# Kernel optimization log

Measured on AMD Instinct MI355X. Metric: run time of the kernel, lower is better.

Reference implementation:

```python
import jax, jax.numpy as jnp
import numpy as np

K = 20          # neighbors
M = 8           # weight-bank size per layer
EPS = 1e-5      # BatchNorm eps


def _bn(x, axes):
    # training-mode BatchNorm at init (gamma=1, beta=0), biased variance like torch
    mu = x.mean(axes, keepdims=True)
    var = x.var(axes, keepdims=True)
    return (x - mu) * jax.lax.rsqrt(var + EPS)


def _gather(feat, idx):
    # feat [B,N,C], idx [B,N,K] -> neighbor features [B,N,K,C]
    return jax.vmap(lambda f, i: f[i])(feat, idx)


def _knn_idx(x):
    # x [B,C,N]; pairwise_distance = -||xi||^2 + 2 xi.xj - ||xj||^2 (neg sq dist)
    sq = jnp.sum(x * x, axis=1)                      # [B,N]
    inner = jnp.einsum('bcn,bcm->bnm', x, x)          # [B,N,N]
    pd = 2.0 * inner - sq[:, :, None] - sq[:, None, :]
    return jax.lax.top_k(pd, K)[1]                    # [B,N,K]


def _scorenet(xyz, w1, w2, b):
    # xyz [B,N,K,6]; 1x1 Conv2d == channel-last matmul; BN2d over (B,N,K)
    h = jax.nn.relu(_bn(xyz @ w1, (0, 1, 2)))         # [B,N,K,16]
    s = h @ w2 + b                                    # [B,N,K,M]
    return jax.nn.softmax(s, axis=-1) + 0.5           # softmax over m, bias=0.5


def _paconv(feat, idx, ker, score):
    # feat [B,N,C]; ker [2C, M*O]; score [B,N,K,M]
    # torch: point = concat(x,x) @ ker -> [B,N,M,O]; center = x @ ker[:C]
    # assemble_dgcnn (assign_score_withk, aggregate='sum'):
    #   out[b,n,o] = sum_{k,m} score[b,n,k,m] * (point[b, idx[b,n,k], m, o] - center[b, n, m, o])
    C = feat.shape[-1]
    k3 = ker.reshape(2 * C, M, -1)
    Wa, Wb = k3[:C], k3[C:]                           # point uses Wa+Wb (x repeated); center uses Wa
    nf = _gather(feat, idx)                           # [B,N,K,C]
    T = jnp.einsum('bnkm,bnkc->bnmc', score, nf)      # score-weighted neighbor feats
    out = jnp.einsum('bnmc,cmo->bno', T, Wa + Wb)
    out = out - jnp.einsum('bnm,bnc,cmo->bno', score.sum(2), feat, Wa)
    return jax.nn.relu(_bn(out, (0, 1)))              # BN1d over (B,N), channel-last


def setup_inputs() -> dict:
    key = jax.random.key(0)
    ks = jax.random.split(key, 18)
    B, N = 32, 1024
    dims = [(3, 64), (64, 64), (64, 128), (128, 256)]
    d = {"x": jax.random.normal(ks[0], (B, 3, N), dtype=jnp.float32)}
    for i, (ci, co) in enumerate(dims):
        scale = (2.0 / (2 * ci)) ** 0.5  # kaiming_normal over fan_in=2*ci
        d[f"mat{i+1}"] = jax.random.normal(ks[1 + i], (2 * ci, M * co), dtype=jnp.float32) * scale
        d[f"sn{i+1}_w1"] = jax.random.normal(ks[5 + i], (6, 16), dtype=jnp.float32) * 0.4
        d[f"sn{i+1}_w2"] = jax.random.normal(ks[9 + i], (16, M), dtype=jnp.float32) * 0.25
        d[f"sn{i+1}_b"] = jnp.zeros((M,), dtype=jnp.float32)
    d["conv5_w"] = jax.random.normal(ks[13], (512, 1024), dtype=jnp.float32) * 0.04
    d["lin1_w"] = jax.random.normal(ks[14], (2048, 512), dtype=jnp.float32) * 0.02
    d["lin2_w"] = jax.random.normal(ks[15], (512, 256), dtype=jnp.float32) * 0.04
    d["lin3_w"] = jax.random.normal(ks[16], (256, 40), dtype=jnp.float32) * 0.06
    d["lin3_b"] = jnp.zeros((40,), dtype=jnp.float32)
    return d


def reference(x, mat1, mat2, mat3, mat4,
              sn1_w1, sn1_w2, sn1_b, sn2_w1, sn2_w2, sn2_b,
              sn3_w1, sn3_w2, sn3_b, sn4_w1, sn4_w2, sn4_b,
              conv5_w, lin1_w, lin2_w, lin3_w, lin3_b):
    idx = _knn_idx(x)                                  # [B,N,K]
    xT = jnp.swapaxes(x, 1, 2)                         # [B,N,3]
    nx = _gather(xT, idx)                              # [B,N,K,3]
    xyz = jnp.concatenate([nx - xT[:, :, None, :], nx], axis=-1)  # [B,N,K,6]

    p1 = _paconv(xT, idx, mat1, _scorenet(xyz, sn1_w1, sn1_w2, sn1_b))  # [B,N,64]
    p2 = _paconv(p1, idx, mat2, _scorenet(xyz, sn2_w1, sn2_w2, sn2_b))  # [B,N,64]
    p3 = _paconv(p2, idx, mat3, _scorenet(xyz, sn3_w1, sn3_w2, sn3_b))  # [B,N,128]
    p4 = _paconv(p3, idx, mat4, _scorenet(xyz, sn4_w1, sn4_w2, sn4_b))  # [B,N,256]

    p = jnp.concatenate([p1, p2, p3, p4], axis=-1)     # [B,N,512]
    p = jax.nn.relu(_bn(p @ conv5_w, (0, 1)))          # [B,N,1024]
    g = jnp.concatenate([p.max(axis=1), p.mean(axis=1)], axis=-1)  # [B,2048]
    h = jax.nn.relu(_bn(g @ lin1_w, (0,)))             # [B,512] (dropout = identity)
    h = jax.nn.relu(_bn(h @ lin2_w, (0,)))             # [B,256]
    return h @ lin3_w + lin3_b                         # [B,40]
```

## Files before the change

### kernel.cpp

```cpp
#include <hip/hip_runtime.h>
#include <cstdint>
#include <cstddef>

static constexpr int Bc  = 32;
static constexpr int Nc  = 1024;
static constexpr int Kc  = 20;
static constexpr int Mc  = 8;
static constexpr int BNc = Bc * Nc;
static constexpr int BNKc = BNc * Kc;

typedef __attribute__((ext_vector_type(4))) float f32x4;
typedef _Float16 f16x8 __attribute__((ext_vector_type(8)));

__device__ inline short f2h(float v) { _Float16 h = (_Float16)v; return __builtin_bit_cast(short, h); }
__device__ inline float h2f(short s) { return (float)__builtin_bit_cast(_Float16, s); }

__global__ void zero_kernel(float* p, int n) {
  int gid = blockIdx.x * blockDim.x + threadIdx.x;
  if (gid < n) p[gid] = 0.f;
}

__global__ __launch_bounds__(256) void knn_kernel(const float* __restrict__ x,
                                                  int* __restrict__ idxout) {
  int wv = threadIdx.x >> 6;
  int bn = blockIdx.x * 4 + wv;
  int b = bn >> 10, n = bn & (Nc - 1);
  int lane = threadIdx.x & 63;
  const float* xb = x + (size_t)b * 3 * Nc;
  float cx = xb[n], cy = xb[Nc + n], cz = xb[2 * Nc + n];
  float sqc = cx * cx + cy * cy + cz * cz;
  float d[16];
#pragma unroll
  for (int j = 0; j < 16; j++) {
    int m2 = j * 64 + lane;
    float xm = xb[m2], ym = xb[Nc + m2], zm = xb[2 * Nc + m2];
    d[j] = 2.f * (cx * xm + cy * ym + cz * zm) - sqc - (xm * xm + ym * ym + zm * zm);
  }
  int* out = idxout + (size_t)bn * Kc;
  for (int kk = 0; kk < Kc; kk++) {
    float bd = d[0]; int bj = 0;
#pragma unroll
    for (int j = 1; j < 16; j++)
      if (d[j] > bd) { bd = d[j]; bj = j; }
    int bm = bj * 64 + lane;
#pragma unroll
    for (int off = 32; off; off >>= 1) {
      float od = __shfl_down(bd, off);
      int   om = __shfl_down(bm, off);
      if (od > bd || (od == bd && om < bm)) { bd = od; bm = om; }
    }
    bm = __shfl(bm, 0);
    if (lane == 0) out[kk] = bm;
    int bmj = bm >> 6;
    bool mine = (bm & 63) == lane;
#pragma unroll
    for (int j = 0; j < 16; j++)
      if (mine && j == bmj) d[j] = -3e38f;
  }
}

__global__ __launch_bounds__(256) void xt_kernel(const float* __restrict__ x,
                                                 float* __restrict__ xT) {
  int gid = blockIdx.x * blockDim.x + threadIdx.x;
  int c = gid % 3;
  int bn = gid / 3;
  int b = bn >> 10, n = bn & (Nc - 1);
  xT[gid] = x[((size_t)b * 3 + c) * Nc + n];
}

__device__ inline void xyz_at(const float* __restrict__ xT, const int* __restrict__ idx,
                              int e, float v[6]) {
  int bn = e / Kc;
  int b = bn >> 10;
  int nb = idx[e];
  const float* pc = xT + (size_t)bn * 3;
  const float* pn = xT + ((size_t)(b << 10) + nb) * 3;
#pragma unroll
  for (int c = 0; c < 3; c++) { float nv = pn[c]; v[c] = nv - pc[c]; v[3 + c] = nv; }
}

__global__ __launch_bounds__(256) void xyz_stats_kernel(const float* __restrict__ xT,
                                                        const int* __restrict__ idx,
                                                        float* __restrict__ accum) {
  __shared__ float sPart[4 * 42];
  int tid = threadIdx.x;
  int gid = blockIdx.x * 256 + tid;
  float a[42];
#pragma unroll
  for (int t = 0; t < 42; t++) a[t] = 0.f;
  for (int i = 0; i < 8; i++) {
    float v[6];
    xyz_at(xT, idx, gid + i * 81920, v);
#pragma unroll
    for (int c = 0; c < 6; c++) a[c] += v[c];
    int t = 6;
#pragma unroll
    for (int c = 0; c < 6; c++)
#pragma unroll
      for (int d = 0; d < 6; d++) a[t++] += v[c] * v[d];
  }
  int lane = tid & 63, wid = tid >> 6;
#pragma unroll
  for (int t = 0; t < 42; t++) {
    float v = a[t];
#pragma unroll
    for (int off = 32; off; off >>= 1) v += __shfl_down(v, off);
    if (lane == 0) sPart[wid * 42 + t] = v;
  }
  __syncthreads();
  if (tid < 42) {
    float s = sPart[tid] + sPart[42 + tid] + sPart[84 + tid] + sPart[126 + tid];
    atomicAdd(&accum[tid], s);
  }
}

__global__ void snstats_kernel(const float* __restrict__ accum,
                               const float* __restrict__ w1a, const float* __restrict__ w1b,
                               const float* __restrict__ w1c, const float* __restrict__ w1d,
                               float* __restrict__ snstats) {
  int t = threadIdx.x;
  int l = t >> 4, j = t & 15;
  const float* w1 = (l == 0) ? w1a : (l == 1) ? w1b : (l == 2) ? w1c : w1d;
  const float invc = 1.f / (float)BNKc;
  float wj[6];
  float mu = 0.f;
#pragma unroll
  for (int c = 0; c < 6; c++) { wj[c] = w1[c * 16 + j]; mu += accum[c] * invc * wj[c]; }
  float e2 = 0.f;
#pragma unroll
  for (int c = 0; c < 6; c++)
#pragma unroll
    for (int d = 0; d < 6; d++) e2 += wj[c] * wj[d] * (accum[6 + c * 6 + d] * invc);
  float var = e2 - mu * mu;
  snstats[t * 2] = mu;
  snstats[t * 2 + 1] = rsqrtf(var + 1e-5f);
}

__global__ __launch_bounds__(256) void score4_kernel(
    const float* __restrict__ xT, const int* __restrict__ idx,
    const float* __restrict__ w1a, const float* __restrict__ w2a, const float* __restrict__ b1,
    const float* __restrict__ w1b, const float* __restrict__ w2b, const float* __restrict__ b2,
    const float* __restrict__ w1c, const float* __restrict__ w2c, const float* __restrict__ b3,
    const float* __restrict__ w1d, const float* __restrict__ w2d, const float* __restrict__ b4,
    const float* __restrict__ snst, short* __restrict__ score4) {
  __shared__ float sW1[4][96], sW2[4][128], sB[4][8], sMu[4][16], sRs[4][16];
  int tid = threadIdx.x;
  if (tid < 96) { sW1[0][tid] = w1a[tid]; sW1[1][tid] = w1b[tid]; sW1[2][tid] = w1c[tid]; sW1[3][tid] = w1d[tid]; }
  else if (tid < 224) { int t = tid - 96; sW2[0][t] = w2a[t]; sW2[1][t] = w2b[t]; sW2[2][t] = w2c[t]; sW2[3][t] = w2d[t]; }
  else if (tid < 232) { int t = tid - 224; sB[0][t] = b1[t]; sB[1][t] = b2[t]; sB[2][t] = b3[t]; sB[3][t] = b4[t]; }
  else if (tid < 248) {
    int t = tid - 232;
#pragma unroll
    for (int l = 0; l < 4; l++) { sMu[l][t] = snst[(l * 16 + t) * 2]; sRs[l][t] = snst[(l * 16 + t) * 2 + 1]; }
  }
  __syncthreads();
  int e = blockIdx.x * 256 + tid;
  float v[6];
  xyz_at(xT, idx, e, v);
#pragma unroll
  for (int l = 0; l < 4; l++) {
    float h[16];
#pragma unroll
    for (int j = 0; j < 16; j++) {
      float a = 0.f;
#pragma unroll
      for (int c = 0; c < 6; c++) a += v[c] * sW1[l][c * 16 + j];
      a = (a - sMu[l][j]) * sRs[l][j];
      h[j] = a > 0.f ? a : 0.f;
    }
    float s[8];
    float mx = -3e38f;
#pragma unroll
    for (int m = 0; m < 8; m++) {
      float a = sB[l][m];
#pragma unroll
      for (int j = 0; j < 16; j++) a += h[j] * sW2[l][j * 8 + m];
      s[m] = a;
      mx = fmaxf(mx, a);
    }
    float sum = 0.f;
#pragma unroll
    for (int m = 0; m < 8; m++) { s[m] = expf(s[m] - mx); sum += s[m]; }
    float inv = 1.f / sum;
    short* op = score4 + (size_t)l * BNKc * 8 + (size_t)e * 8;
#pragma unroll
    for (int m = 0; m < 8; m++) op[m] = f2h(s[m] * inv + 0.5f);
  }
}

template <int C, int Co, int MH>
__global__ __launch_bounds__(256) void paconv_kernel(
    const float* __restrict__ feat, int fstride,
    const float* __restrict__ ker,
    const short* __restrict__ score,
    const int* __restrict__ idx,
    float* __restrict__ outp, int ostride) {
  constexpr int PT = 8;
  constexpr int MS = Mc / MH;
  __shared__ float sX[PT][2 * MH * C];
  __shared__ float sSc[PT * Kc * Mc];
  __shared__ int sIdx[PT * Kc];
  __shared__ float sFc[PT][C];
  __shared__ float sSum[PT][Mc];

  int tid = threadIdx.x;
  int pbase = blockIdx.x * PT;
  int bN = pbase & ~(Nc - 1);

  for (int e = tid; e < PT * Kc; e += 256) sIdx[e] = idx[(size_t)pbase * Kc + e];
  for (int e = tid; e < PT * Kc * Mc; e += 256) sSc[e] = h2f(score[(size_t)pbase * Kc * Mc + e]);
  for (int e = tid; e < PT * C; e += 256) {
    int p = e / C, c = e - p * C;
    sFc[p][c] = feat[(size_t)(pbase + p) * fstride + c];
  }
  __syncthreads();
  for (int e = tid; e < PT * Mc; e += 256) {
    int p = e >> 3, m = e & 7;
    float s = 0.f;
#pragma unroll
    for (int k = 0; k < Kc; k++) s += sSc[p * Kc * Mc + k * Mc + m];
    sSum[p][m] = s;
  }
  __syncthreads();

  constexpr int OG = Co;
  constexpr int PG = 256 / OG;
  constexpr int PPT = PT / PG;
  int o = tid % OG;
  int pg = tid / OG;
  float acc[PPT];
#pragma unroll
  for (int i = 0; i < PPT; i++) acc[i] = 0.f;

  for (int ms = 0; ms < MS; ms++) {
    int mb = ms * MH;
    for (int e = tid; e < PT * C; e += 256) {
      int p = e / C, c = e - p * C;
      float t[MH];
#pragma unroll
      for (int mm = 0; mm < MH; mm++) t[mm] = 0.f;
      const float* sc = &sSc[p * Kc * Mc + mb];
      for (int k = 0; k < Kc; k++) {
        float v = feat[(size_t)(bN + sIdx[p * Kc + k]) * fstride + c];
#pragma unroll
        for (int mm = 0; mm < MH; mm++) t[mm] += sc[k * Mc + mm] * v;
      }
      float fc = sFc[p][c];
#pragma unroll
      for (int mm = 0; mm < MH; mm++) {
        sX[p][mm * C + c] = t[mm] - sSum[p][mb + mm] * fc;
        sX[p][MH * C + mm * C + c] = t[mm];
      }
    }
    __syncthreads();
#pragma unroll
    for (int mm = 0; mm < MH; mm++) {
      int m = mb + mm;
      const float* kerm = ker + (size_t)m * Co + o;
      for (int c = 0; c < C; c++) {
        float wA = kerm[(size_t)c * (Mc * Co)];
        float wB = kerm[(size_t)(C + c) * (Mc * Co)];
        int r = mm * C + c;
#pragma unroll
        for (int i = 0; i < PPT; i++) {
          int p = pg * PPT + i;
          acc[i] += sX[p][r] * wA;
          acc[i] += sX[p][MH * C + r] * wB;
        }
      }
    }
    __syncthreads();
  }

#pragma unroll
  for (int i = 0; i < PPT; i++) {
    int p = pg * PPT + i;
    outp[(size_t)(pbase + p) * ostride + o] = acc[i];
  }
}

template <int C>
__global__ __launch_bounds__(256) void gather_kernel(
    const short* __restrict__ pb, int coff,
    const short* __restrict__ score,
    const int* __restrict__ idx,
    short* __restrict__ T, short* __restrict__ sumb) {
  constexpr int PT = 256 / C;
  constexpr int KH = Mc * C;
  __shared__ float sSc[PT][Kc][Mc];
  __shared__ int   sIdx[PT][Kc];
  int tid = threadIdx.x;
  int pbase = blockIdx.x * PT;
  int bbase = pbase & ~(Nc - 1);
  for (int e = tid; e < PT * Kc * Mc; e += 256) (&sSc[0][0][0])[e] = h2f(score[(size_t)pbase * Kc * Mc + e]);
  for (int e = tid; e < PT * Kc; e += 256) (&sIdx[0][0])[e] = idx[(size_t)pbase * Kc + e];
  __syncthreads();
  if (tid < PT * Mc) {
    int p = tid >> 3, m = tid & 7;
    float s = 0.f;
#pragma unroll
    for (int k = 0; k < Kc; k++) s += sSc[p][k][m];
    sumb[(size_t)(pbase + p) * 8 + m] = f2h(s);
  }
  int p = tid / C, c = tid - p * C;
  float t[Mc];
#pragma unroll
  for (int m = 0; m < Mc; m++) t[m] = 0.f;
  for (int k = 0; k < Kc; k++) {
    float v = h2f(pb[(size_t)(bbase + sIdx[p][k]) * 512 + coff + c]);
#pragma unroll
    for (int m = 0; m < Mc; m++) t[m] += sSc[p][k][m] * v;
  }
  short* rowp = T + (size_t)(pbase + p) * KH;
#pragma unroll
  for (int m = 0; m < Mc; m++) rowp[m * C + c] = f2h(t[m]);
}

__global__ __launch_bounds__(256) void kerconv_all_kernel(
    const float* __restrict__ m2, const float* __restrict__ m3,
    const float* __restrict__ m4, const float* __restrict__ w5,
    short* __restrict__ kb) {
  int gid = blockIdx.x * 256 + threadIdx.x;
  const float* ker; short* dst; int C, Co, g;
  if (gid < 65536)       { ker = m2; dst = kb;          C = 64;  Co = 64;  g = gid; }
  else if (gid < 196608) { ker = m3; dst = kb + 65536;  C = 64;  Co = 128; g = gid - 65536; }
  else if (gid < 720896) { ker = m4; dst = kb + 196608; C = 128; Co = 256; g = gid - 196608; }
  else {
    int g5 = gid - 720896;
    int o = g5 >> 9, k = g5 & 511;
    kb[720896 + g5] = f2h(w5[(size_t)k * 1024 + o]);
    return;
  }
  int KH = Mc * C, K2 = 2 * KH;
  int o = g / K2, r = g - o * K2;
  float v;
  if (r < KH) {
    int m = r / C, c = r - m * C;
    v = ker[(size_t)c * (Mc * Co) + m * Co + o] + ker[(size_t)(C + c) * (Mc * Co) + m * Co + o];
  } else {
    int r2 = r - KH;
    int m = r2 / C, c = r2 - m * C;
    v = -ker[(size_t)c * (Mc * Co) + m * Co + o];
  }
  dst[g] = f2h(v);
}

template <int BM, int BN, bool OUT_HALF>
__global__ __launch_bounds__(256) void gemm_kernel(
    const short* __restrict__ A,
    const short* __restrict__ Bt,
    int K,
    void* __restrict__ Cout, int ldc) {
  constexpr int BK = 64;
  constexpr int FN = BN / 32;
  constexpr int FMW = BM / 32;
  __shared__ short sA[BM * BK];
  __shared__ short sB[BN * BK];
  int tid = threadIdx.x;
  int lane = tid & 63, wv = tid >> 6;
  int wrow = (wv & 1) * (BM / 2);
  int wcol = (wv >> 1) * (BN / 2);
  int bm0 = blockIdx.x * BM;
  int bn0 = blockIdx.y * BN;
  int r15 = lane & 15, quad = lane >> 4;
  int swz = r15 & 7;

  f32x4 acc[FMW][FN];
#pragma unroll
  for (int fm = 0; fm < FMW; fm++)
#pragma unroll
    for (int fn = 0; fn < FN; fn++) acc[fm][fn] = (f32x4){0.f, 0.f, 0.f, 0.f};

  for (int k0 = 0; k0 < K; k0 += BK) {
#pragma unroll
    for (int i = 0; i < (BM * BK / 8) / 256; i++) {
      int cb = i * 256 + wv * 64;
      int chunk = cb + lane;
      int row = chunk >> 3, kc = (chunk & 7) ^ (row & 7);
      const short* g = A + (size_t)(bm0 + row) * K + k0 + kc * 8;
      __builtin_amdgcn_global_load_lds((const __attribute__((address_space(1))) void*)g,
                                       (__attribute__((address_space(3))) void*)&sA[cb * 8],
                                       16, 0, 0);
    }
#pragma unroll
    for (int i = 0; i < (BN * BK / 8) / 256; i++) {
      int cb = i * 256 + wv * 64;
      int chunk = cb + lane;
      int row = chunk >> 3, kc = (chunk & 7) ^ (row & 7);
      const short* g = Bt + (size_t)(bn0 + row) * K + k0 + kc * 8;
      __builtin_amdgcn_global_load_lds((const __attribute__((address_space(1))) void*)g,
                                       (__attribute__((address_space(3))) void*)&sB[cb * 8],
                                       16, 0, 0);
    }
    __syncthreads();
#pragma unroll
    for (int kk = 0; kk < BK; kk += 32) {
      f16x8 af[FMW], bf[FN];
      int ccol = (kk >> 3) + quad;
#pragma unroll
      for (int fm = 0; fm < FMW; fm++)
        af[fm] = *(const f16x8*)&sA[(wrow + fm * 16 + r15) * BK + ((ccol ^ swz) * 8)];
#pragma unroll
      for (int fn = 0; fn < FN; fn++)
        bf[fn] = *(const f16x8*)&sB[(wcol + fn * 16 + r15) * BK + ((ccol ^ swz) * 8)];
#pragma unroll
      for (int fm = 0; fm < FMW; fm++)
#pragma unroll
        for (int fn = 0; fn < FN; fn++)
          acc[fm][fn] = __builtin_amdgcn_mfma_f32_16x16x32_f16(af[fm], bf[fn], acc[fm][fn], 0, 0, 0);
    }
    __syncthreads();
  }

#pragma unroll
  for (int fn = 0; fn < FN; fn++) {
    int col = bn0 + wcol + fn * 16 + r15;
#pragma unroll
    for (int fm = 0; fm < FMW; fm++) {
      int rowb = bm0 + wrow + fm * 16 + quad * 4;
#pragma unroll
      for (int r = 0; r < 4; r++) {
        float v = acc[fm][fn][r];
        if constexpr (OUT_HALF) ((short*)Cout)[(size_t)(rowb + r) * ldc + col] = f2h(v);
        else                    ((float*)Cout)[(size_t)(rowb + r) * ldc + col] = v;
      }
    }
  }
}

template <int BM, int BN, int C>
__global__ __launch_bounds__(256) void gemm_r1_kernel(
    const short* __restrict__ T,
    const short* __restrict__ Bt,
    const short* __restrict__ pb, int coff,
    const short* __restrict__ sumb,
    short* __restrict__ Cout, int ldc) {
  constexpr int BK = 64;
  constexpr int KH = Mc * C;
  constexpr int K2 = 2 * KH;
  constexpr int FN = BN / 32;
  constexpr int FMW = BM / 32;
  __shared__ short sA[BM * BK];
  __shared__ short sB[BN * BK];
  __shared__ short sFc[BM * C];
  __shared__ short sSm[BM * 8];
  int tid = threadIdx.x;
  int lane = tid & 63, wv = tid >> 6;
  int wrow = (wv & 1) * (BM / 2);
  int wcol = (wv >> 1) * (BN / 2);
  int bm0 = blockIdx.x * BM;
  int bn0 = blockIdx.y * BN;
  int r15 = lane & 15, quad = lane >> 4;
  int swz = r15 & 7;

  for (int e = tid; e < BM * C; e += 256) {
    int p = e / C, c = e - p * C;
    sFc[e] = pb[(size_t)(bm0 + p) * 512 + coff + c];
  }
  for (int e = tid; e < BM * 8; e += 256) sSm[e] = sumb[(size_t)bm0 * 8 + e];

  f32x4 acc[FMW][FN];
#pragma unroll
  for (int fm = 0; fm < FMW; fm++)
#pragma unroll
    for (int fn = 0; fn < FN; fn++) acc[fm][fn] = (f32x4){0.f, 0.f, 0.f, 0.f};
  __syncthreads();

  for (int k0 = 0; k0 < K2; k0 += BK) {
    if (k0 < KH) {
#pragma unroll
      for (int i = 0; i < (BM * BK / 8) / 256; i++) {
        int cb = i * 256 + wv * 64;
        int chunk = cb + lane;
        int row = chunk >> 3, kc = (chunk & 7) ^ (row & 7);
        const short* g = T + (size_t)(bm0 + row) * KH + k0 + kc * 8;
        __builtin_amdgcn_global_load_lds((const __attribute__((address_space(1))) void*)g,
                                         (__attribute__((address_space(3))) void*)&sA[cb * 8],
                                         16, 0, 0);
      }
    } else {
#pragma unroll
      for (int i = 0; i < (BM * BK / 8) / 256; i++) {
        int cb = i * 256 + wv * 64;
        int chunk = cb + lane;
        int row = chunk >> 3, kc = (chunk & 7) ^ (row & 7);
        int kb = (k0 - KH) + kc * 8;
        int m = kb / C, c = kb - m * C;
        _Float16 sm = __builtin_bit_cast(_Float16, sSm[row * 8 + m]);
        f16x8 fcv = *(const f16x8*)&sFc[row * C + c];
        f16x8 val;
#pragma unroll
        for (int j = 0; j < 8; j++) val[j] = sm * fcv[j];
        *(f16x8*)&sA[chunk * 8] = val;
      }
    }
#pragma unroll
    for (int i = 0; i < (BN * BK / 8) / 256; i++) {
      int cb = i * 256 + wv * 64;
      int chunk = cb + lane;
      int row = chunk >> 3, kc = (chunk & 7) ^ (row & 7);
      const short* g = Bt + (size_t)(bn0 + row) * K2 + k0 + kc * 8;
      __builtin_amdgcn_global_load_lds((const __attribute__((address_space(1))) void*)g,
                                       (__attribute__((address_space(3))) void*)&sB[cb * 8],
                                       16, 0, 0);
    }
    __syncthreads();
#pragma unroll
    for (int kk = 0; kk < BK; kk += 32) {
      f16x8 af[FMW], bf[FN];
      int ccol = (kk >> 3) + quad;
#pragma unroll
      for (int fm = 0; fm < FMW; fm++)
        af[fm] = *(const f16x8*)&sA[(wrow + fm * 16 + r15) * BK + ((ccol ^ swz) * 8)];
#pragma unroll
      for (int fn = 0; fn < FN; fn++)
        bf[fn] = *(const f16x8*)&sB[(wcol + fn * 16 + r15) * BK + ((ccol ^ swz) * 8)];
#pragma unroll
      for (int fm = 0; fm < FMW; fm++)
#pragma unroll
        for (int fn = 0; fn < FN; fn++)
          acc[fm][fn] = __builtin_amdgcn_mfma_f32_16x16x32_f16(af[fm], bf[fn], acc[fm][fn], 0, 0, 0);
    }
    __syncthreads();
  }

#pragma unroll
  for (int fn = 0; fn < FN; fn++) {
    int col = bn0 + wcol + fn * 16 + r15;
#pragma unroll
    for (int fm = 0; fm < FMW; fm++) {
      int rowb = bm0 + wrow + fm * 16 + quad * 4;
#pragma unroll
      for (int r = 0; r < 4; r++)
        Cout[(size_t)(rowb + r) * ldc + col] = f2h(acc[fm][fn][r]);
    }
  }
}

template <bool IS_HALF>
__global__ __launch_bounds__(256) void bnstats_kernel(const void* __restrict__ pre,
                                                      int Co,
                                                      float* __restrict__ bnslots) {
  __shared__ float sS[4][64], sQ[4][64];
  int tid = threadIdx.x;
  int c = tid & 63, tg = tid >> 6;
  int ch = blockIdx.x * 64 + c;
  int row0 = blockIdx.y * 1024 + tg * 256;
  float s = 0.f, q = 0.f;
  if constexpr (IS_HALF) {
    const short* p = (const short*)pre + (size_t)row0 * Co + ch;
#pragma unroll 4
    for (int r = 0; r < 256; r++) {
      float v = h2f(p[(size_t)r * Co]);
      s += v; q += v * v;
    }
  } else {
    const float* p = (const float*)pre + (size_t)row0 * Co + ch;
#pragma unroll 4
    for (int r = 0; r < 256; r++) {
      float v = p[(size_t)r * Co];
      s += v; q += v * v;
    }
  }
  sS[tg][c] = s; sQ[tg][c] = q;
  __syncthreads();
  if (tid < 64) {
    float ts = sS[0][tid] + sS[1][tid] + sS[2][tid] + sS[3][tid];
    float tq = sQ[0][tid] + sQ[1][tid] + sQ[2][tid] + sQ[3][tid];
    int chh = blockIdx.x * 64 + tid;
    bnslots[(chh * 32 + blockIdx.y) * 2 + 0] = ts;
    bnslots[(chh * 32 + blockIdx.y) * 2 + 1] = tq;
  }
}

__global__ void bnfinalize_kernel(const float* __restrict__ slots,
                                  float* __restrict__ bnmr, int Co) {
  int ch = blockIdx.x * blockDim.x + threadIdx.x;
  if (ch >= Co) return;
  float s = 0.f, q = 0.f;
#pragma unroll 4
  for (int i = 0; i < 32; i++) { s += slots[(ch * 32 + i) * 2]; q += slots[(ch * 32 + i) * 2 + 1]; }
  float mu = s / (float)BNc;
  float var = q / (float)BNc - mu * mu;
  bnmr[ch * 2] = mu;
  bnmr[ch * 2 + 1] = rsqrtf(var + 1e-5f);
}

__global__ __launch_bounds__(256) void bnapply_kernel(const float* __restrict__ pre,
                                                      int Co, const float* __restrict__ bnmr,
                                                      short* __restrict__ pb, int coff) {
  int gid = blockIdx.x * 256 + threadIdx.x;
  int row = gid / Co, ch = gid - row * Co;
  float mu = bnmr[ch * 2], rs = bnmr[ch * 2 + 1];
  float v = (pre[gid] - mu) * rs;
  pb[(size_t)row * 512 + coff + ch] = f2h(v > 0.f ? v : 0.f);
}

__global__ __launch_bounds__(256) void bnapply16_kernel(const short* __restrict__ pre,
                                                        int Co, const float* __restrict__ bnmr,
                                                        short* __restrict__ pb, int coff) {
  int gid = blockIdx.x * 256 + threadIdx.x;
  int row = gid / Co, ch = gid - row * Co;
  float mu = bnmr[ch * 2], rs = bnmr[ch * 2 + 1];
  float v = (h2f(pre[gid]) - mu) * rs;
  pb[(size_t)row * 512 + coff + ch] = f2h(v > 0.f ? v : 0.f);
}

__global__ __launch_bounds__(512) void g2_kernel(const short* __restrict__ pre,
                                                 const float* __restrict__ bnmr,
                                                 float* __restrict__ g) {
  int b = blockIdx.x, nch = blockIdx.y;
  int tid = threadIdx.x;
  int ch0 = 2 * tid;
  float mu0 = bnmr[ch0 * 2],     rs0 = bnmr[ch0 * 2 + 1];
  float mu1 = bnmr[ch0 * 2 + 2], rs1 = bnmr[ch0 * 2 + 3];
  const uint32_t* p32 = (const uint32_t*)(pre + (size_t)b * 1024 * 1024 + (size_t)nch * 128 * 1024);
  float mx0 = 0.f, mx1 = 0.f, sm0 = 0.f, sm1 = 0.f;
#pragma unroll 4
  for (int n = 0; n < 128; n++) {
    uint32_t u = p32[n * 512 + tid];
    float v0 = (h2f((short)(u & 0xffff)) - mu0) * rs0;
    float v1 = (h2f((short)(u >> 16))    - mu1) * rs1;
    v0 = v0 > 0.f ? v0 : 0.f;
    v1 = v1 > 0.f ? v1 : 0.f;
    mx0 = fmaxf(mx0, v0); mx1 = fmaxf(mx1, v1);
    sm0 += v0; sm1 += v1;
  }
  int* gi = (int*)g;
  atomicMax(&gi[b * 2048 + ch0], __float_as_int(mx0));
  atomicMax(&gi[b * 2048 + ch0 + 1], __float_as_int(mx1));
  atomicAdd(&g[b * 2048 + 1024 + ch0], sm0 * (1.f / 1024.f));
  atomicAdd(&g[b * 2048 + 1024 + ch0 + 1], sm1 * (1.f / 1024.f));
}

__global__ __launch_bounds__(256) void linsplit_kernel(const float* __restrict__ A,
                                                       const float* __restrict__ W,
                                                       float* __restrict__ out,
                                                       int Kdim, int Cols, int kchunk) {
  int j = blockIdx.x * 256 + threadIdx.x;
  if (j >= Cols) return;
  int b = blockIdx.y;
  int k0 = blockIdx.z * kchunk;
  const float* a = A + (size_t)b * Kdim + k0;
  const float* w = W + (size_t)k0 * Cols + j;
  float acc = 0.f;
#pragma unroll 4
  for (int i = 0; i < kchunk; i++) acc += a[i] * w[(size_t)i * Cols];
  atomicAdd(&out[b * Cols + j], acc);
}

__global__ __launch_bounds__(256) void biasinit_kernel(const float* __restrict__ bias,
                                                       float* __restrict__ out, int Cols, int n) {
  int gid = blockIdx.x * 256 + threadIdx.x;
  if (gid < n) out[gid] = bias[gid % Cols];
}

__global__ __launch_bounds__(256) void lin_bn_kernel(float* __restrict__ X, int Cols) {
  int j = blockIdx.x * 256 + threadIdx.x;
  if (j >= Cols) return;
  float s = 0.f, q = 0.f;
#pragma unroll
  for (int b = 0; b < 32; b++) { float v = X[b * Cols + j]; s += v; q += v * v; }
  float mu = s * (1.f / 32.f);
  float var = q * (1.f / 32.f) - mu * mu;
  float rs = rsqrtf(var + 1e-5f);
#pragma unroll
  for (int b = 0; b < 32; b++) {
    float v = (X[b * Cols + j] - mu) * rs;
    X[b * Cols + j] = v > 0.f ? v : 0.f;
  }
}

extern "C" void kernel_launch(void* const* d_in, const int* in_sizes, int n_in,
                              void* d_out, int out_size, void* d_ws, size_t ws_size,
                              hipStream_t stream) {
  (void)in_sizes; (void)n_in; (void)out_size; (void)ws_size;
  const float* x      = (const float*)d_in[0];
  const float* mat1   = (const float*)d_in[1];
  const float* sn1_w1 = (const float*)d_in[2];
  const float* sn1_w2 = (const float*)d_in[3];
  const float* sn1_b  = (const float*)d_in[4];
  const float* mat2   = (const float*)d_in[5];
  const float* sn2_w1 = (const float*)d_in[6];
  const float* sn2_w2 = (const float*)d_in[7];
  const float* sn2_b  = (const float*)d_in[8];
  const float* mat3   = (const float*)d_in[9];
  const float* sn3_w1 = (const float*)d_in[10];
  const float* sn3_w2 = (const float*)d_in[11];
  const float* sn3_b  = (const float*)d_in[12];
  const float* mat4   = (const float*)d_in[13];
  const float* sn4_w1 = (const float*)d_in[14];
  const float* sn4_w2 = (const float*)d_in[15];
  const float* sn4_b  = (const float*)d_in[16];
  const float* conv5w = (const float*)d_in[17];
  const float* lin1w  = (const float*)d_in[18];
  const float* lin2w  = (const float*)d_in[19];
  const float* lin3w  = (const float*)d_in[20];
  const float* lin3b  = (const float*)d_in[21];
  float* out = (float*)d_out;

  char* ws = (char*)d_ws;
  size_t cur = 0;
  auto alloc = [&](size_t bytes) {
    size_t r = cur;
    cur += (bytes + 1023) & ~(size_t)1023;
    return r;
  };
  size_t off_idx   = alloc((size_t)BNKc * 4);
  size_t off_xT    = alloc((size_t)BNc * 3 * 4);
  size_t off_st    = alloc((size_t)157888 * 4);
  size_t off_sum   = alloc((size_t)BNc * 8 * 2);
  size_t off_score = alloc((size_t)BNKc * 8 * 2 * 4);
  size_t off_pre   = alloc((size_t)BNc * 256 * 4);
  size_t off_pb    = alloc((size_t)BNc * 512 * 2);
  size_t off_kb    = alloc((size_t)1245184 * 2);
  size_t off_TU    = alloc((size_t)BNc * 1024 * 2);

  int*   idx    = (int*)(ws + off_idx);
  float* xT     = (float*)(ws + off_xT);
  float* stats  = (float*)(ws + off_st);
  short* sumb   = (short*)(ws + off_sum);
  short* score4 = (short*)(ws + off_score);
  float* pre    = (float*)(ws + off_pre);
  short* pre16  = (short*)(ws + off_pre);
  short* pb     = (short*)(ws + off_pb);
  short* kb     = (short*)(ws + off_kb);
  short* T      = (short*)(ws + off_TU);
  short* pre5   = (short*)(ws + off_TU);

  float* xyzacc  = stats;
  float* snstats = stats + 64;
  float* bnslots = stats + 192;
  float* bnmr    = stats + 65728;
  float* g       = stats + 67776;
  float* h1      = stats + 133312;
  float* h2      = stats + 149696;

  zero_kernel<<<1, 64, 0, stream>>>(xyzacc, 64);
  knn_kernel<<<BNc / 4, 256, 0, stream>>>(x, idx);
  xt_kernel<<<BNc * 3 / 256, 256, 0, stream>>>(x, xT);
  xyz_stats_kernel<<<320, 256, 0, stream>>>(xT, idx, xyzacc);
  snstats_kernel<<<1, 64, 0, stream>>>(xyzacc, sn1_w1, sn2_w1, sn3_w1, sn4_w1, snstats);

  score4_kernel<<<BNKc / 256, 256, 0, stream>>>(
      xT, idx, sn1_w1, sn1_w2, sn1_b, sn2_w1, sn2_w2, sn2_b,
      sn3_w1, sn3_w2, sn3_b, sn4_w1, sn4_w2, sn4_b, snstats, score4);
  kerconv_all_kernel<<<4864, 256, 0, stream>>>(mat2, mat3, mat4, conv5w, kb);

  short* sc1 = score4;
  short* sc2 = score4 + (size_t)1 * BNKc * 8;
  short* sc3 = score4 + (size_t)2 * BNKc * 8;
  short* sc4 = score4 + (size_t)3 * BNKc * 8;
  short* kbL2 = kb;
  short* kbL3 = kb + 65536;
  short* kbL4 = kb + 196608;
  short* kbW5 = kb + 720896;

  paconv_kernel<3, 64, 8><<<BNc / 8, 256, 0, stream>>>(xT, 3, mat1, sc1, idx, pre, 64);
  bnstats_kernel<false><<<dim3(1, 32), 256, 0, stream>>>(pre, 64, bnslots);
  bnfinalize_kernel<<<1, 64, 0, stream>>>(bnslots, bnmr, 64);
  bnapply_kernel<<<BNc * 64 / 256, 256, 0, stream>>>(pre, 64, bnmr, pb, 0);

  gather_kernel<64><<<BNc / 4, 256, 0, stream>>>(pb, 0, sc2, idx, T, sumb);
  gemm_r1_kernel<64, 64, 64><<<dim3(512, 1), 256, 0, stream>>>(T, kbL2, pb, 0, sumb, pre16, 64);
  bnstats_kernel<true><<<dim3(1, 32), 256, 0, stream>>>(pre16, 64, bnslots);
  bnfinalize_kernel<<<1, 64, 0, stream>>>(bnslots, bnmr, 64);
  bnapply16_kernel<<<BNc * 64 / 256, 256, 0, stream>>>(pre16, 64, bnmr, pb, 64);

  gather_kernel<64><<<BNc / 4, 256, 0, stream>>>(pb, 64, sc3, idx, T, sumb);
  gemm_r1_kernel<64, 128, 64><<<dim3(512, 1), 256, 0, stream>>>(T, kbL3, pb, 64, sumb, pre16, 128);
  bnstats_kernel<true><<<dim3(2, 32), 256, 0, stream>>>(pre16, 128, bnslots);
  bnfinalize_kernel<<<1, 128, 0, stream>>>(bnslots, bnmr, 128);
  bnapply16_kernel<<<BNc * 128 / 256, 256, 0, stream>>>(pre16, 128, bnmr, pb, 128);

  gather_kernel<128><<<BNc / 2, 256, 0, stream>>>(pb, 128, sc4, idx, T, sumb);
  gemm_r1_kernel<64, 128, 128><<<dim3(512, 2), 256, 0, stream>>>(T, kbL4, pb, 128, sumb, pre16, 256);
  bnstats_kernel<true><<<dim3(4, 32), 256, 0, stream>>>(pre16, 256, bnslots);
  bnfinalize_kernel<<<1, 256, 0, stream>>>(bnslots, bnmr, 256);
  bnapply16_kernel<<<BNc * 256 / 256, 256, 0, stream>>>(pre16, 256, bnmr, pb, 256);

  gemm_kernel<128, 128, true><<<dim3(256, 8), 256, 0, stream>>>(pb, kbW5, 512, pre5, 1024);
  bnstats_kernel<true><<<dim3(16, 32), 256, 0, stream>>>(pre5, 1024, bnslots);
  bnfinalize_kernel<<<4, 256, 0, stream>>>(bnslots, bnmr, 1024);

  zero_kernel<<<256, 256, 0, stream>>>(g, 65536);
  g2_kernel<<<dim3(32, 8), 512, 0, stream>>>(pre5, bnmr, g);

  zero_kernel<<<64, 256, 0, stream>>>(h1, 16384);
  linsplit_kernel<<<dim3(2, 32, 8), 256, 0, stream>>>(g, lin1w, h1, 2048, 512, 256);
  lin_bn_kernel<<<2, 256, 0, stream>>>(h1, 512);
  zero_kernel<<<32, 256, 0, stream>>>(h2, 8192);
  linsplit_kernel<<<dim3(1, 32, 4), 256, 0, stream>>>(h1, lin2w, h2, 512, 256, 128);
  lin_bn_kernel<<<1, 256, 0, stream>>>(h2, 256);
  biasinit_kernel<<<5, 256, 0, stream>>>(lin3b, out, 40, 1280);
  linsplit_kernel<<<dim3(1, 32, 2), 256, 0, stream>>>(h2, lin3w, out, 256, 40, 128);
}
```

Measured before the change: 780.4 us.

## Fold small kernels to cut launches and replace atomics with deterministic reductions

Folds the xT transpose into the knn kernel and drops the separate transpose and zero-fill launches. The xyz statistics now write per-block partials that snstats reduces, instead of using atomics. Global max/mean pooling becomes a single block per (batch, channel group) with a shared-memory reduction in place of atomics, so g no longer needs zeroing. The last linear layer becomes one kernel that adds the bias directly. The aim is fewer launches and less atomic traffic, at the cost of narrower 16-bit strided loads in the pooling kernel.

```diff
diff --git a/kernel.cpp b/kernel.cpp
--- a/kernel.cpp
+++ b/kernel.cpp
@@ -21,13 +21,19 @@
 }
 
 __global__ __launch_bounds__(256) void knn_kernel(const float* __restrict__ x,
-                                                  int* __restrict__ idxout) {
+                                                  int* __restrict__ idxout,
+                                                  float* __restrict__ xT) {
   int wv = threadIdx.x >> 6;
   int bn = blockIdx.x * 4 + wv;
   int b = bn >> 10, n = bn & (Nc - 1);
   int lane = threadIdx.x & 63;
   const float* xb = x + (size_t)b * 3 * Nc;
   float cx = xb[n], cy = xb[Nc + n], cz = xb[2 * Nc + n];
+  if (lane == 0) {
+    xT[(size_t)bn * 3 + 0] = cx;
+    xT[(size_t)bn * 3 + 1] = cy;
+    xT[(size_t)bn * 3 + 2] = cz;
+  }
   float sqc = cx * cx + cy * cy + cz * cz;
   float d[16];
 #pragma unroll
@@ -57,15 +63,6 @@
     for (int j = 0; j < 16; j++)
       if (mine && j == bmj) d[j] = -3e38f;
   }
-}
-
-__global__ __launch_bounds__(256) void xt_kernel(const float* __restrict__ x,
-                                                 float* __restrict__ xT) {
-  int gid = blockIdx.x * blockDim.x + threadIdx.x;
-  int c = gid % 3;
-  int bn = gid / 3;
-  int b = bn >> 10, n = bn & (Nc - 1);
-  xT[gid] = x[((size_t)b * 3 + c) * Nc + n];
 }
 
 __device__ inline void xyz_at(const float* __restrict__ xT, const int* __restrict__ idx,
@@ -81,7 +78,7 @@
 
 __global__ __launch_bounds__(256) void xyz_stats_kernel(const float* __restrict__ xT,
                                                         const int* __restrict__ idx,
-                                                        float* __restrict__ accum) {
+                                                        float* __restrict__ parts) {
   __shared__ float sPart[4 * 42];
   int tid = threadIdx.x;
   int gid = blockIdx.x * 256 + tid;
@@ -108,29 +105,34 @@
     if (lane == 0) sPart[wid * 42 + t] = v;
   }
   __syncthreads();
-  if (tid < 42) {
-    float s = sPart[tid] + sPart[42 + tid] + sPart[84 + tid] + sPart[126 + tid];
-    atomicAdd(&accum[tid], s);
-  }
-}
-
-__global__ void snstats_kernel(const float* __restrict__ accum,
+  if (tid < 42)
+    parts[blockIdx.x * 42 + tid] = sPart[tid] + sPart[42 + tid] + sPart[84 + tid] + sPart[126 + tid];
+}
+
+__global__ void snstats_kernel(const float* __restrict__ parts,
                                const float* __restrict__ w1a, const float* __restrict__ w1b,
                                const float* __restrict__ w1c, const float* __restrict__ w1d,
                                float* __restrict__ snstats) {
+  __shared__ float sAcc[42];
   int t = threadIdx.x;
+  if (t < 42) {
+    float s = 0.f;
+    for (int i = 0; i < 320; i++) s += parts[i * 42 + t];
+    sAcc[t] = s;
+  }
+  __syncthreads();
   int l = t >> 4, j = t & 15;
   const float* w1 = (l == 0) ? w1a : (l == 1) ? w1b : (l == 2) ? w1c : w1d;
   const float invc = 1.f / (float)BNKc;
   float wj[6];
   float mu = 0.f;
 #pragma unroll
-  for (int c = 0; c < 6; c++) { wj[c] = w1[c * 16 + j]; mu += accum[c] * invc * wj[c]; }
+  for (int c = 0; c < 6; c++) { wj[c] = w1[c * 16 + j]; mu += sAcc[c] * invc * wj[c]; }
   float e2 = 0.f;
 #pragma unroll
   for (int c = 0; c < 6; c++)
 #pragma unroll
-    for (int d = 0; d < 6; d++) e2 += wj[c] * wj[d] * (accum[6 + c * 6 + d] * invc);
+    for (int d = 0; d < 6; d++) e2 += wj[c] * wj[d] * (sAcc[6 + c * 6 + d] * invc);
   float var = e2 - mu * mu;
   snstats[t * 2] = mu;
   snstats[t * 2 + 1] = rsqrtf(var + 1e-5f);
@@ -606,31 +608,32 @@
   pb[(size_t)row * 512 + coff + ch] = f2h(v > 0.f ? v : 0.f);
 }
 
-__global__ __launch_bounds__(512) void g2_kernel(const short* __restrict__ pre,
+__global__ __launch_bounds__(512) void g3_kernel(const short* __restrict__ pre,
                                                  const float* __restrict__ bnmr,
                                                  float* __restrict__ g) {
-  int b = blockIdx.x, nch = blockIdx.y;
+  __shared__ float sMx[4][128], sSm[4][128];
+  int b = blockIdx.x, cg = blockIdx.y;
   int tid = threadIdx.x;
-  int ch0 = 2 * tid;
-  float mu0 = bnmr[ch0 * 2],     rs0 = bnmr[ch0 * 2 + 1];
-  float mu1 = bnmr[ch0 * 2 + 2], rs1 = bnmr[ch0 * 2 + 3];
-  const uint32_t* p32 = (const uint32_t*)(pre + (size_t)b * 1024 * 1024 + (size_t)nch * 128 * 1024);
-  float mx0 = 0.f, mx1 = 0.f, sm0 = 0.f, sm1 = 0.f;
+  int cl = tid & 127, rg = tid >> 7;
+  int ch = cg * 128 + cl;
+  float mu = bnmr[ch * 2], rs = bnmr[ch * 2 + 1];
+  const short* base = pre + (size_t)b * 1024 * 1024 + (size_t)rg * 256 * 1024 + ch;
+  float mx = 0.f, sm = 0.f;
 #pragma unroll 4
-  for (int n = 0; n < 128; n++) {
-    uint32_t u = p32[n * 512 + tid];
-    float v0 = (h2f((short)(u & 0xffff)) - mu0) * rs0;
-    float v1 = (h2f((short)(u >> 16))    - mu1) * rs1;
-    v0 = v0 > 0.f ? v0 : 0.f;
-    v1 = v1 > 0.f ? v1 : 0.f;
-    mx0 = fmaxf(mx0, v0); mx1 = fmaxf(mx1, v1);
-    sm0 += v0; sm1 += v1;
-  }
-  int* gi = (int*)g;
-  atomicMax(&gi[b * 2048 + ch0], __float_as_int(mx0));
-  atomicMax(&gi[b * 2048 + ch0 + 1], __float_as_int(mx1));
-  atomicAdd(&g[b * 2048 + 1024 + ch0], sm0 * (1.f / 1024.f));
-  atomicAdd(&g[b * 2048 + 1024 + ch0 + 1], sm1 * (1.f / 1024.f));
+  for (int n = 0; n < 256; n++) {
+    float v = (h2f(base[(size_t)n * 1024]) - mu) * rs;
+    v = v > 0.f ? v : 0.f;
+    mx = fmaxf(mx, v);
+    sm += v;
+  }
+  sMx[rg][cl] = mx; sSm[rg][cl] = sm;
+  __syncthreads();
+  if (rg == 0) {
+    float m0 = fmaxf(fmaxf(sMx[0][cl], sMx[1][cl]), fmaxf(sMx[2][cl], sMx[3][cl]));
+    float s0 = sSm[0][cl] + sSm[1][cl] + sSm[2][cl] + sSm[3][cl];
+    g[b * 2048 + ch] = m0;
+    g[b * 2048 + 1024 + ch] = s0 * (1.f / 1024.f);
+  }
 }
 
 __global__ __launch_bounds__(256) void linsplit_kernel(const float* __restrict__ A,
@@ -649,10 +652,18 @@
   atomicAdd(&out[b * Cols + j], acc);
 }
 
-__global__ __launch_bounds__(256) void biasinit_kernel(const float* __restrict__ bias,
-                                                       float* __restrict__ out, int Cols, int n) {
-  int gid = blockIdx.x * 256 + threadIdx.x;
-  if (gid < n) out[gid] = bias[gid % Cols];
+__global__ __launch_bounds__(64) void lin3_kernel(const float* __restrict__ A,
+                                                  const float* __restrict__ W,
+                                                  const float* __restrict__ bias,
+                                                  float* __restrict__ out) {
+  int j = threadIdx.x;
+  if (j >= 40) return;
+  int b = blockIdx.y;
+  const float* a = A + (size_t)b * 256;
+  float acc = bias[j];
+#pragma unroll 4
+  for (int i = 0; i < 256; i++) acc += a[i] * W[(size_t)i * 40 + j];
+  out[b * 40 + j] = acc;
 }
 
 __global__ __launch_bounds__(256) void lin_bn_kernel(float* __restrict__ X, int Cols) {
@@ -708,7 +719,7 @@
   };
   size_t off_idx   = alloc((size_t)BNKc * 4);
   size_t off_xT    = alloc((size_t)BNc * 3 * 4);
-  size_t off_st    = alloc((size_t)157888 * 4);
+  size_t off_st    = alloc((size_t)200000 * 4);
   size_t off_sum   = alloc((size_t)BNc * 8 * 2);
   size_t off_score = alloc((size_t)BNKc * 8 * 2 * 4);
   size_t off_pre   = alloc((size_t)BNc * 256 * 4);
@@ -728,19 +739,17 @@
   short* T      = (short*)(ws + off_TU);
   short* pre5   = (short*)(ws + off_TU);
 
-  float* xyzacc  = stats;
-  float* snstats = stats + 64;
-  float* bnslots = stats + 192;
-  float* bnmr    = stats + 65728;
-  float* g       = stats + 67776;
-  float* h1      = stats + 133312;
-  float* h2      = stats + 149696;
-
-  zero_kernel<<<1, 64, 0, stream>>>(xyzacc, 64);
-  knn_kernel<<<BNc / 4, 256, 0, stream>>>(x, idx);
-  xt_kernel<<<BNc * 3 / 256, 256, 0, stream>>>(x, xT);
-  xyz_stats_kernel<<<320, 256, 0, stream>>>(xT, idx, xyzacc);
-  snstats_kernel<<<1, 64, 0, stream>>>(xyzacc, sn1_w1, sn2_w1, sn3_w1, sn4_w1, snstats);
+  float* parts   = stats;
+  float* snstats = stats + 13504;
+  float* bnslots = stats + 13632;
+  float* bnmr    = stats + 79168;
+  float* g       = stats + 81216;
+  float* h1      = stats + 146752;
+  float* h2      = stats + 163136;
+
+  knn_kernel<<<BNc / 4, 256, 0, stream>>>(x, idx, xT);
+  xyz_stats_kernel<<<320, 256, 0, stream>>>(xT, idx, parts);
+  snstats_kernel<<<1, 64, 0, stream>>>(parts, sn1_w1, sn2_w1, sn3_w1, sn4_w1, snstats);
 
   score4_kernel<<<BNKc / 256, 256, 0, stream>>>(
       xT, idx, sn1_w1, sn1_w2, sn1_b, sn2_w1, sn2_w2, sn2_b,
@@ -783,8 +792,7 @@
   bnstats_kernel<true><<<dim3(16, 32), 256, 0, stream>>>(pre5, 1024, bnslots);
   bnfinalize_kernel<<<4, 256, 0, stream>>>(bnslots, bnmr, 1024);
 
-  zero_kernel<<<256, 256, 0, stream>>>(g, 65536);
-  g2_kernel<<<dim3(32, 8), 512, 0, stream>>>(pre5, bnmr, g);
+  g3_kernel<<<dim3(32, 8), 512, 0, stream>>>(pre5, bnmr, g);
 
   zero_kernel<<<64, 256, 0, stream>>>(h1, 16384);
   linsplit_kernel<<<dim3(2, 32, 8), 256, 0, stream>>>(g, lin1w, h1, 2048, 512, 256);
@@ -792,6 +800,5 @@
   zero_kernel<<<32, 256, 0, stream>>>(h2, 8192);
   linsplit_kernel<<<dim3(1, 32, 4), 256, 0, stream>>>(h1, lin2w, h2, 512, 256, 128);
   lin_bn_kernel<<<1, 256, 0, stream>>>(h2, 256);
-  biasinit_kernel<<<5, 256, 0, stream>>>(lin3b, out, 40, 1280);
-  linsplit_kernel<<<dim3(1, 32, 2), 256, 0, stream>>>(h2, lin3w, out, 256, 40, 128);
-}
+  lin3_kernel<<<dim3(1, 32), 64, 0, stream>>>(h2, lin3w, lin3b, out);
+}
```

Result: slower. 813.1 us (+4.2%).
